# Performance work log

Measured on AMD Instinct MI355X. Metric: run time of the kernel, lower is better.

The kernel has to match this reference:

```python
import jax, jax.numpy as jnp
import numpy as np

S, B, D, H = 256, 32, 512, 512

def setup_inputs() -> dict:
    key = jax.random.key(0)
    ks = jax.random.split(key, 14)
    return {
        "x": jax.random.normal(ks[0], (S, B, D), jnp.float32),
        "hidden_prev": jax.random.normal(ks[1], (1, B, H), jnp.float32) * 0.1,
        "Z_state": jax.random.normal(ks[2], (1, B, H, D), jnp.float32) * 0.01,
        "F_state": jax.random.normal(ks[3], (1, B, H, D), jnp.float32) * 0.01,
        "wz_state": jax.random.normal(ks[4], (1, B, H), jnp.float32) * 0.01,
        "wf_state": jax.random.normal(ks[5], (1, B, H), jnp.float32) * 0.01,
        "bz_state": jax.random.normal(ks[6], (1, B, H), jnp.float32) * 0.01,
        "bf_state": jax.random.normal(ks[7], (1, B, H), jnp.float32) * 0.01,
        "wm_z": jax.random.normal(ks[8], (H, D), jnp.float32) * 0.1,
        "wm_f": jax.random.normal(ks[9], (H, D), jnp.float32) * 0.1,
        "wv_z": jax.random.normal(ks[10], (1, H), jnp.float32) * 0.1,
        "wv_f": jax.random.normal(ks[11], (1, H), jnp.float32) * 0.1,
        "bias_z": jax.random.normal(ks[12], (1, H), jnp.float32) * 0.1,
        "bias_f": jax.random.normal(ks[13], (1, H), jnp.float32) * 0.1,
    }

def reference(x, hidden_prev, Z_state, F_state, wz_state, wf_state, bz_state, bf_state,
              wm_z, wm_f, wv_z, wv_f, bias_z, bias_f):
    # Input projections for both gates, done once: [S,B,H]
    pre_z = jnp.einsum('sbd,hd->sbh', x, wm_z)
    pre_f = jnp.einsum('sbd,hd->sbh', x, wm_f)

    def step(carry, inp):
        cell, Z, Fm, wz, wf, bz, bf = carry
        x_t, pz, pf = inp  # [B,D], [B,H], [B,H]
        z = jnp.tanh(pz + wv_z * cell + bias_z)          # [B,H]
        f = jax.nn.sigmoid(pf + wv_f * cell + bias_f)    # [B,H]
        zf = (1.0 - f) * (1.0 - z * z)
        fz = (cell - z) * (1.0 - f) * f
        common = f + zf * wv_z + fz * wv_f
        # RTRL sensitivity updates (outer products over [B,H,D])
        Zn = common[..., None] * Z + zf[..., None] * x_t[:, None, :]
        Fn = common[..., None] * Fm + fz[..., None] * x_t[:, None, :]
        wzn = cell * zf + common * wz
        wfn = cell * fz + common * wf
        bzn = zf + common * bz
        bfn = fz + common * bf
        new_cell = cell * f + (1.0 - f) * z
        return (new_cell, Zn, Fn, wzn, wfn, bzn, bfn), new_cell

    carry0 = (hidden_prev[0], Z_state[0], F_state[0],
              wz_state[0], wf_state[0], bz_state[0], bf_state[0])
    carry, cells = jax.lax.scan(step, carry0, (x, pre_z, pre_f))
    new_cell, Zn, Fn, wzn, wfn, bzn, bfn = carry
    return (cells, new_cell[None], Zn[None], Fn[None],
            wzn[None], wfn[None], bzn[None], bfn[None])
```

## Files before the change

kernel.cpp:

```cpp
#include <hip/hip_runtime.h>
#include <math.h>

namespace {

typedef short short8 __attribute__((ext_vector_type(8)));
typedef float floatx4 __attribute__((ext_vector_type(4)));
typedef unsigned int uint32;
typedef unsigned short u16;
typedef unsigned long long u64;

constexpr int S = 256, B = 32, D = 512, H = 512;
constexpr int BH = B * H;
constexpr int M1 = S * B;
constexpr int WN = H * D;
constexpr int SBH = S * BH;

__device__ __forceinline__ int swz(int row, int col8) {
  return row * 64 + (col8 ^ ((row & 7) << 3));
}

__device__ __forceinline__ uint32 f2bf(float f) {
  uint32 x = __float_as_uint(f);
  return (x + 0x7fffu + ((x >> 16) & 1u)) >> 16;
}

__device__ __forceinline__ float fast_sigmoid(float x) {
  float e = __expf(-x);
  return __builtin_amdgcn_rcpf(1.0f + e);
}
__device__ __forceinline__ float fast_tanh(float x) {
  float e = __expf(-2.0f * x);
  return fmaf(2.0f, __builtin_amdgcn_rcpf(1.0f + e), -1.0f);
}

__global__ __launch_bounds__(256) void prep_kernel(
    const float* __restrict__ x, const float* __restrict__ wmz,
    const float* __restrict__ wmf, u16* __restrict__ XT,
    u16* __restrict__ wmzb, u16* __restrict__ wmfb) {
  __shared__ float lds[64][65];
  const int bid = blockIdx.x;
  if (bid < 1024) {
    const int b = bid >> 5;
    const int rem = bid & 31;
    const int d0 = (rem >> 2) * 64;
    const int s0 = (rem & 3) * 64;
    const int r = threadIdx.x >> 4;
    const int c4 = (threadIdx.x & 15) * 4;
#pragma unroll
    for (int p = 0; p < 4; ++p) {
      const int rr = r + p * 16;
      float4 v = *(const float4*)&x[(size_t)(s0 + rr) * (B * D) +
                                    (size_t)b * D + d0 + c4];
      lds[c4 + 0][rr] = v.x;
      lds[c4 + 1][rr] = v.y;
      lds[c4 + 2][rr] = v.z;
      lds[c4 + 3][rr] = v.w;
    }
    __syncthreads();
#pragma unroll
    for (int p = 0; p < 4; ++p) {
      const int dr = r + p * 16;
      const float v0 = lds[dr][c4 + 0];
      const float v1 = lds[dr][c4 + 1];
      const float v2 = lds[dr][c4 + 2];
      const float v3 = lds[dr][c4 + 3];
      u64 o = (u64)f2bf(v0) | ((u64)f2bf(v1) << 16) | ((u64)f2bf(v2) << 32) |
              ((u64)f2bf(v3) << 48);
      *(u64*)&XT[((size_t)b * D + d0 + dr) * S + s0 + c4] = o;
    }
  } else {
    int i = ((bid - 1024) * 256 + threadIdx.x) * 8;
    const float* src;
    u16* dst;
    int off;
    if (i < WN) {
      src = wmz; dst = wmzb; off = i;
    } else {
      src = wmf; dst = wmfb; off = i - WN;
    }
    float4 a = *(const float4*)&src[off];
    float4 b4 = *(const float4*)&src[off + 4];
    uint4 o;
    o.x = f2bf(a.x) | (f2bf(a.y) << 16);
    o.y = f2bf(a.z) | (f2bf(a.w) << 16);
    o.z = f2bf(b4.x) | (f2bf(b4.y) << 16);
    o.w = f2bf(b4.z) | (f2bf(b4.w) << 16);
    *(uint4*)&dst[off] = o;
  }
}

__global__ __launch_bounds__(256) void proj_gemm(
    const float* __restrict__ x, const u16* __restrict__ wmzb,
    const u16* __restrict__ wmfb, float2* __restrict__ pzf) {
  __shared__ u16 As[128 * 64];
  __shared__ u16 Bzs[64 * 64];
  __shared__ u16 Bfs[64 * 64];
  const int tid = threadIdx.x;
  const int m0 = blockIdx.x * 128;
  const int n0 = blockIdx.y * 64;
  const int w = tid >> 6, l = tid & 63;
  const int lr = l & 15, lg = l >> 4;
  floatx4 accz[2][4], accf[2][4];
#pragma unroll
  for (int m = 0; m < 2; ++m)
#pragma unroll
    for (int n = 0; n < 4; ++n) {
      accz[m][n] = 0;
      accf[m][n] = 0;
    }
  const int sr = tid >> 3;
  const int sc = (tid & 7) * 8;
  for (int k0 = 0; k0 < D; k0 += 64) {
    __syncthreads();
#pragma unroll
    for (int p = 0; p < 4; ++p) {
      const int r = sr + 32 * p;
      const float* xp = &x[(size_t)(m0 + r) * D + k0 + sc];
      float4 a = *(const float4*)xp;
      float4 b = *(const float4*)(xp + 4);
      uint4 o;
      o.x = f2bf(a.x) | (f2bf(a.y) << 16);
      o.y = f2bf(a.z) | (f2bf(a.w) << 16);
      o.z = f2bf(b.x) | (f2bf(b.y) << 16);
      o.w = f2bf(b.z) | (f2bf(b.w) << 16);
      *(uint4*)&As[swz(r, sc)] = o;
    }
#pragma unroll
    for (int p = 0; p < 2; ++p) {
      const int r = sr + 32 * p;
      *(short8*)&Bzs[swz(r, sc)] =
          *(const short8*)&wmzb[(size_t)(n0 + r) * D + k0 + sc];
      *(short8*)&Bfs[swz(r, sc)] =
          *(const short8*)&wmfb[(size_t)(n0 + r) * D + k0 + sc];
    }
    __syncthreads();
    __builtin_amdgcn_s_setprio(1);
#pragma unroll
    for (int kk = 0; kk < 2; ++kk) {
      const int kb = kk * 32 + lg * 8;
      short8 a0 = *(const short8*)&As[swz(32 * w + lr, kb)];
      short8 a1 = *(const short8*)&As[swz(32 * w + 16 + lr, kb)];
#pragma unroll
      for (int n = 0; n < 4; ++n) {
        short8 bz = *(const short8*)&Bzs[swz(16 * n + lr, kb)];
        short8 bf = *(const short8*)&Bfs[swz(16 * n + lr, kb)];
        accz[0][n] = __builtin_amdgcn_mfma_f32_16x16x32_bf16(a0, bz, accz[0][n], 0, 0, 0);
        accz[1][n] = __builtin_amdgcn_mfma_f32_16x16x32_bf16(a1, bz, accz[1][n], 0, 0, 0);
        accf[0][n] = __builtin_amdgcn_mfma_f32_16x16x32_bf16(a0, bf, accf[0][n], 0, 0, 0);
        accf[1][n] = __builtin_amdgcn_mfma_f32_16x16x32_bf16(a1, bf, accf[1][n], 0, 0, 0);
      }
    }
    __builtin_amdgcn_s_setprio(0);
  }
#pragma unroll
  for (int m = 0; m < 2; ++m)
#pragma unroll
    for (int n = 0; n < 4; ++n)
#pragma unroll
      for (int j = 0; j < 4; ++j) {
        int row = m0 + 32 * w + 16 * m + lg * 4 + j;
        int col = n0 + 16 * n + lr;
        pzf[(size_t)row * H + col] = make_float2(accz[m][n][j], accf[m][n][j]);
      }
}

#define STEP_BODY(J)                                                       \
    const float z = fast_tanh(fmaf(wvz, cell, pzv));                       \
    const float f = fast_sigmoid(fmaf(wvf, cell, pfv));                    \
    const float zf = (1.0f - f) * (1.0f - z * z);                          \
    const float fz = (cell - z) * (1.0f - f) * f;                          \
    const float common = f + zf * wvz + fz * wvf;                          \
    wz = fmaf(common, wz, cell * zf);                                      \
    wf = fmaf(common, wf, cell * fz);                                      \
    bz = fmaf(common, bz, zf);                                             \
    bf = fmaf(common, bf, fz);                                             \
    cell = fmaf(f, cell - z, z);                                           \
    const size_t ti = (size_t)(t0 + (J)) * BH;                             \
    cp[ti] = cell;                                                         \
    pz[ti] = make_float2(                                                  \
        __uint_as_float(f2bf(zf) | (f2bf(fz) << 16)), common);

#define STEP_L(J, Q)                                                       \
  {                                                                        \
    const float pzv = Q.x + bsz, pfv = Q.y + bsf;                          \
    Q = pz[(size_t)(t0 + 16 + (J)) * BH];                                  \
    STEP_BODY(J)                                                           \
  }

#define STEP_N(J, Q)                                                       \
  {                                                                        \
    const float pzv = Q.x + bsz, pfv = Q.y + bsf;                          \
    STEP_BODY(J)                                                           \
  }

__global__ __launch_bounds__(64, 1) void scan_fwd(
    const float* __restrict__ hidden_prev, const float* __restrict__ wz0,
    const float* __restrict__ wf0, const float* __restrict__ bz0,
    const float* __restrict__ bf0, const float* __restrict__ wvz_,
    const float* __restrict__ wvf_, const float* __restrict__ bsz_,
    const float* __restrict__ bsf_, float2* pzf_,
    float* __restrict__ out_cells, float* __restrict__ out_newcell,
    float* __restrict__ out_wzn, float* __restrict__ out_wfn,
    float* __restrict__ out_bzn, float* __restrict__ out_bfn) {
  const int bh = blockIdx.x * 64 + threadIdx.x;
  const int h = bh & (H - 1);
  float cell = hidden_prev[bh];
  float wz = wz0[bh], wf = wf0[bh], bz = bz0[bh], bf = bf0[bh];
  const float wvz = wvz_[h], wvf = wvf_[h], bsz = bsz_[h], bsf = bsf_[h];
  float2* pz = pzf_ + bh;
  float* cp = out_cells + bh;

  float2 q0 = pz[(size_t)0 * BH], q1 = pz[(size_t)1 * BH];
  float2 q2 = pz[(size_t)2 * BH], q3 = pz[(size_t)3 * BH];
  float2 q4 = pz[(size_t)4 * BH], q5 = pz[(size_t)5 * BH];
  float2 q6 = pz[(size_t)6 * BH], q7 = pz[(size_t)7 * BH];
  float2 q8 = pz[(size_t)8 * BH], q9 = pz[(size_t)9 * BH];
  float2 q10 = pz[(size_t)10 * BH], q11 = pz[(size_t)11 * BH];
  float2 q12 = pz[(size_t)12 * BH], q13 = pz[(size_t)13 * BH];
  float2 q14 = pz[(size_t)14 * BH], q15 = pz[(size_t)15 * BH];

  for (int t0 = 0; t0 < S - 16; t0 += 16) {
    STEP_L(0, q0)  STEP_L(1, q1)  STEP_L(2, q2)  STEP_L(3, q3)
    STEP_L(4, q4)  STEP_L(5, q5)  STEP_L(6, q6)  STEP_L(7, q7)
    STEP_L(8, q8)  STEP_L(9, q9)  STEP_L(10, q10) STEP_L(11, q11)
    STEP_L(12, q12) STEP_L(13, q13) STEP_L(14, q14) STEP_L(15, q15)
  }
  {
    const int t0 = S - 16;
    STEP_N(0, q0)  STEP_N(1, q1)  STEP_N(2, q2)  STEP_N(3, q3)
    STEP_N(4, q4)  STEP_N(5, q5)  STEP_N(6, q6)  STEP_N(7, q7)
    STEP_N(8, q8)  STEP_N(9, q9)  STEP_N(10, q10) STEP_N(11, q11)
    STEP_N(12, q12) STEP_N(13, q13) STEP_N(14, q14) STEP_N(15, q15)
  }
  out_newcell[bh] = cell;
  out_wzn[bh] = wz;
  out_wfn[bh] = wf;
  out_bzn[bh] = bz;
  out_bfn[bh] = bf;
}

__global__ __launch_bounds__(1024) void suffix_kernel(
    const float2* __restrict__ pzfc, u16* __restrict__ AzT,
    u16* __restrict__ AfT, float* __restrict__ P0_out) {
  __shared__ float prods[16][65];
  __shared__ uint32 tl[S * 65];
  const int bh_l = threadIdx.x & 63;
  const int c = threadIdx.x >> 6;
  const int bh = blockIdx.x * 64 + bh_l;
  const float2* p = pzfc + bh;
  float2 v[16];
#pragma unroll
  for (int i = 0; i < 16; ++i) v[i] = p[(size_t)(c * 16 + i) * BH];
  float L = 1.0f;
#pragma unroll
  for (int i = 0; i < 16; ++i) L *= v[i].y;
  prods[c][bh_l] = L;
  __syncthreads();
  float run = 1.0f;
#pragma unroll
  for (int cc = 1; cc < 16; ++cc)
    if (cc > c) run *= prods[cc][bh_l];
#pragma unroll
  for (int i = 15; i >= 0; --i) {
    const int t = c * 16 + i;
    const uint32 w32 = __float_as_uint(v[i].x);
    const float zf = __uint_as_float((w32 & 0xffffu) << 16);
    const float fz = __uint_as_float(w32 & 0xffff0000u);
    tl[t * 65 + bh_l] = f2bf(zf * run) | (f2bf(fz * run) << 16);
    run *= v[i].y;
  }
  if (c == 0) P0_out[bh] = run;
  __syncthreads();
  const size_t base = (size_t)blockIdx.x * 64 * S;
#pragma unroll
  for (int it = 0; it < 4; ++it) {
    const int qi = it * 1024 + threadIdx.x;
    const int r = qi >> 6;
    const int qt = (qi & 63) * 4;
    const uint32 a0 = tl[(qt + 0) * 65 + r];
    const uint32 a1 = tl[(qt + 1) * 65 + r];
    const uint32 a2 = tl[(qt + 2) * 65 + r];
    const uint32 a3 = tl[(qt + 3) * 65 + r];
    u64 lo = (u64)(a0 & 0xffffu) | ((u64)(a1 & 0xffffu) << 16) |
             ((u64)(a2 & 0xffffu) << 32) | ((u64)(a3 & 0xffffu) << 48);
    u64 hi = (u64)(a0 >> 16) | ((u64)(a1 >> 16) << 16) |
             ((u64)(a2 >> 16) << 32) | ((u64)(a3 >> 16) << 48);
    *(u64*)&AzT[base + (size_t)r * S + qt] = lo;
    *(u64*)&AfT[base + (size_t)r * S + qt] = hi;
  }
}

__global__ __launch_bounds__(256, 3) void out_gemm(
    const u16* __restrict__ AzT, const u16* __restrict__ AfT,
    const u16* __restrict__ XT, const float* __restrict__ P0,
    const float* __restrict__ Z0, const float* __restrict__ F0,
    float* __restrict__ Zn, float* __restrict__ Fn) {
  __shared__ u16 smem[2][(128 + 64) * 64];
  const int tid = threadIdx.x;
  const int h0 = blockIdx.x * 128;
  const int d0 = blockIdx.y * 64;
  const int bz = blockIdx.z;
  const int b = bz >> 1;
  const u16* A = ((bz & 1) ? AfT : AzT) + (size_t)b * H * S;
  const float* C0 = (bz & 1) ? F0 : Z0;
  float* Cn = (bz & 1) ? Fn : Zn;
  const u16* Xb = XT + (size_t)b * D * S;
  const int w = tid >> 6, l = tid & 63;
  const int lr = l & 15, lg = l >> 4;
  floatx4 acc[2][4];
#pragma unroll
  for (int m = 0; m < 2; ++m)
#pragma unroll
    for (int n = 0; n < 4; ++n) acc[m][n] = 0;
  const int sr = tid >> 3;
  const int sc = (tid & 7) * 8;

  short8 rA[4], rX[2];

#define OG_LOAD(T0)                                                        \
  {                                                                        \
    _Pragma("unroll") for (int p = 0; p < 4; ++p) {                        \
      const int r = sr + 32 * p;                                           \
      rA[p] = *(const short8*)&A[(size_t)(h0 + r) * S + (T0) + sc];        \
    }                                                                      \
    _Pragma("unroll") for (int p = 0; p < 2; ++p) {                        \
      const int r = sr + 32 * p;                                           \
      rX[p] = *(const short8*)&Xb[(size_t)(d0 + r) * S + (T0) + sc];       \
    }                                                                      \
  }

#define OG_WRITE(BUF)                                                      \
  {                                                                        \
    u16* As_ = smem[BUF];                                                  \
    u16* Xs_ = smem[BUF] + 128 * 64;                                       \
    _Pragma("unroll") for (int p = 0; p < 4; ++p) {                        \
      const int r = sr + 32 * p;                                           \
      *(short8*)&As_[swz(r, sc)] = rA[p];                                  \
    }                                                                      \
    _Pragma("unroll") for (int p = 0; p < 2; ++p) {                        \
      const int r = sr + 32 * p;                                           \
      *(short8*)&Xs_[swz(r, sc)] = rX[p];                                  \
    }                                                                      \
  }

#define OG_COMPUTE(BUF)                                                    \
  {                                                                        \
    const u16* As_ = smem[BUF];                                            \
    const u16* Xs_ = smem[BUF] + 128 * 64;                                 \
    __builtin_amdgcn_s_setprio(1);                                         \
    _Pragma("unroll") for (int kk = 0; kk < 2; ++kk) {                     \
      const int kb = kk * 32 + lg * 8;                                     \
      short8 a0 = *(const short8*)&As_[swz(32 * w + lr, kb)];              \
      short8 a1 = *(const short8*)&As_[swz(32 * w + 16 + lr, kb)];         \
      _Pragma("unroll") for (int n = 0; n < 4; ++n) {                      \
        short8 xf = *(const short8*)&Xs_[swz(16 * n + lr, kb)];            \
        acc[0][n] = __builtin_amdgcn_mfma_f32_16x16x32_bf16(a0, xf, acc[0][n], 0, 0, 0); \
        acc[1][n] = __builtin_amdgcn_mfma_f32_16x16x32_bf16(a1, xf, acc[1][n], 0, 0, 0); \
      }                                                                    \
    }                                                                      \
    __builtin_amdgcn_s_setprio(0);                                         \
  }

  OG_LOAD(0)
  OG_WRITE(0)
  __syncthreads();
  OG_LOAD(64)
  OG_COMPUTE(0)
  OG_WRITE(1)
  __syncthreads();
  OG_LOAD(128)
  OG_COMPUTE(1)
  OG_WRITE(0)
  __syncthreads();
  OG_LOAD(192)
  OG_COMPUTE(0)
  OG_WRITE(1)
  __syncthreads();

  float4 c0v[8];
  float p0v[8];
#pragma unroll
  for (int i = 0; i < 8; ++i) {
    const int id = i * 256 + tid;
    const int row = id >> 4;
    const int c4 = (id & 15) * 4;
    const int h = h0 + row;
    p0v[i] = P0[b * H + h];
    c0v[i] = *(const float4*)&C0[((size_t)b * H + h) * D + d0 + c4];
  }

  OG_COMPUTE(1)

  __syncthreads();
  float* eps = (float*)&smem[0][0];
#pragma unroll
  for (int m = 0; m < 2; ++m)
#pragma unroll
    for (int n = 0; n < 4; ++n)
#pragma unroll
      for (int j = 0; j < 4; ++j) {
        const int row = 32 * w + 16 * m + lg * 4 + j;
        eps[row * 68 + 16 * n + lr] = acc[m][n][j];
      }
  __syncthreads();
#pragma unroll
  for (int i = 0; i < 8; ++i) {
    const int id = i * 256 + tid;
    const int row = id >> 4;
    const int c4 = (id & 15) * 4;
    const int h = h0 + row;
    const size_t gi = ((size_t)b * H + h) * D + d0 + c4;
    const float4 a = *(const float4*)&eps[row * 68 + c4];
    float4 o;
    o.x = fmaf(p0v[i], c0v[i].x, a.x);
    o.y = fmaf(p0v[i], c0v[i].y, a.y);
    o.z = fmaf(p0v[i], c0v[i].z, a.z);
    o.w = fmaf(p0v[i], c0v[i].w, a.w);
    *(float4*)&Cn[gi] = o;
  }
#undef OG_LOAD
#undef OG_WRITE
#undef OG_COMPUTE
}

}

extern "C" void kernel_launch(void* const* d_in, const int* in_sizes, int n_in,
                              void* d_out, int out_size, void* d_ws,
                              size_t ws_size, hipStream_t stream) {
  const float* x = (const float*)d_in[0];
  const float* hidden_prev = (const float*)d_in[1];
  const float* Z_state = (const float*)d_in[2];
  const float* F_state = (const float*)d_in[3];
  const float* wz_state = (const float*)d_in[4];
  const float* wf_state = (const float*)d_in[5];
  const float* bz_state = (const float*)d_in[6];
  const float* bf_state = (const float*)d_in[7];
  const float* wm_z = (const float*)d_in[8];
  const float* wm_f = (const float*)d_in[9];
  const float* wv_z = (const float*)d_in[10];
  const float* wv_f = (const float*)d_in[11];
  const float* bias_z = (const float*)d_in[12];
  const float* bias_f = (const float*)d_in[13];

  float2* pzf = (float2*)d_ws;
  u16* AzT = (u16*)(pzf + SBH);
  u16* AfT = AzT + SBH;
  u16* XT = AfT + SBH;
  u16* wmzb = XT + SBH;
  u16* wmfb = wmzb + WN;
  float* P0 = (float*)(wmfb + WN);

  float* out = (float*)d_out;
  float* out_cells = out;
  float* out_newcell = out + SBH;
  float* out_Zn = out_newcell + BH;
  float* out_Fn = out_Zn + (size_t)BH * D;
  float* out_wzn = out_Fn + (size_t)BH * D;
  float* out_wfn = out_wzn + BH;
  float* out_bzn = out_wfn + BH;
  float* out_bfn = out_bzn + BH;

  prep_kernel<<<1024 + 256, 256, 0, stream>>>(x, wm_z, wm_f, XT, wmzb, wmfb);
  proj_gemm<<<dim3(M1 / 128, H / 64), 256, 0, stream>>>(x, wmzb, wmfb, pzf);
  scan_fwd<<<BH / 64, 64, 0, stream>>>(
      hidden_prev, wz_state, wf_state, bz_state, bf_state, wv_z, wv_f, bias_z,
      bias_f, pzf, out_cells, out_newcell, out_wzn, out_wfn, out_bzn,
      out_bfn);
  suffix_kernel<<<BH / 64, 1024, 0, stream>>>(pzf, AzT, AfT, P0);
  out_gemm<<<dim3(H / 128, D / 64, B * 2), 256, 0, stream>>>(
      AzT, AfT, XT, P0, Z_state, F_state, out_Zn, out_Fn);
}
```

Baseline: 101.9 us.

## Drop prep kernel: convert weights in GEMM, fuse x transpose into suffix kernel

Removes the separate prep kernel. proj_gemm now loads fp32 weights and converts them to bf16 in-kernel, and the x transpose-to-bf16 (XT) is folded into suffix_kernel, reusing its LDS through a union. The bf16 conversion switches to the packed __float22bfloat162_rn intrinsic, and the LDS transpose reads are rotated to reduce bank conflicts. This saves one launch and the bf16 weight staging buffers, but each proj_gemm block now re-reads and re-converts fp32 weights and suffix_kernel does extra work before its main phase.

```diff
diff --git a/kernel.cpp b/kernel.cpp
--- a/kernel.cpp
+++ b/kernel.cpp
@@ -1,4 +1,5 @@
 #include <hip/hip_runtime.h>
+#include <hip/hip_bf16.h>
 #include <math.h>
 
 namespace {
@@ -12,16 +13,17 @@
 constexpr int S = 256, B = 32, D = 512, H = 512;
 constexpr int BH = B * H;
 constexpr int M1 = S * B;
-constexpr int WN = H * D;
 constexpr int SBH = S * BH;
 
 __device__ __forceinline__ int swz(int row, int col8) {
   return row * 64 + (col8 ^ ((row & 7) << 3));
 }
 
-__device__ __forceinline__ uint32 f2bf(float f) {
-  uint32 x = __float_as_uint(f);
-  return (x + 0x7fffu + ((x >> 16) & 1u)) >> 16;
+__device__ __forceinline__ uint32 pkbf(float lo, float hi) {
+  __hip_bfloat162 h = __float22bfloat162_rn(make_float2(lo, hi));
+  uint32 r;
+  __builtin_memcpy(&r, &h, 4);
+  return r;
 }
 
 __device__ __forceinline__ float fast_sigmoid(float x) {
@@ -33,65 +35,9 @@
   return fmaf(2.0f, __builtin_amdgcn_rcpf(1.0f + e), -1.0f);
 }
 
-__global__ __launch_bounds__(256) void prep_kernel(
+__global__ __launch_bounds__(256) void proj_gemm(
     const float* __restrict__ x, const float* __restrict__ wmz,
-    const float* __restrict__ wmf, u16* __restrict__ XT,
-    u16* __restrict__ wmzb, u16* __restrict__ wmfb) {
-  __shared__ float lds[64][65];
-  const int bid = blockIdx.x;
-  if (bid < 1024) {
-    const int b = bid >> 5;
-    const int rem = bid & 31;
-    const int d0 = (rem >> 2) * 64;
-    const int s0 = (rem & 3) * 64;
-    const int r = threadIdx.x >> 4;
-    const int c4 = (threadIdx.x & 15) * 4;
-#pragma unroll
-    for (int p = 0; p < 4; ++p) {
-      const int rr = r + p * 16;
-      float4 v = *(const float4*)&x[(size_t)(s0 + rr) * (B * D) +
-                                    (size_t)b * D + d0 + c4];
-      lds[c4 + 0][rr] = v.x;
-      lds[c4 + 1][rr] = v.y;
-      lds[c4 + 2][rr] = v.z;
-      lds[c4 + 3][rr] = v.w;
-    }
-    __syncthreads();
-#pragma unroll
-    for (int p = 0; p < 4; ++p) {
-      const int dr = r + p * 16;
-      const float v0 = lds[dr][c4 + 0];
-      const float v1 = lds[dr][c4 + 1];
-      const float v2 = lds[dr][c4 + 2];
-      const float v3 = lds[dr][c4 + 3];
-      u64 o = (u64)f2bf(v0) | ((u64)f2bf(v1) << 16) | ((u64)f2bf(v2) << 32) |
-              ((u64)f2bf(v3) << 48);
-      *(u64*)&XT[((size_t)b * D + d0 + dr) * S + s0 + c4] = o;
-    }
-  } else {
-    int i = ((bid - 1024) * 256 + threadIdx.x) * 8;
-    const float* src;
-    u16* dst;
-    int off;
-    if (i < WN) {
-      src = wmz; dst = wmzb; off = i;
-    } else {
-      src = wmf; dst = wmfb; off = i - WN;
-    }
-    float4 a = *(const float4*)&src[off];
-    float4 b4 = *(const float4*)&src[off + 4];
-    uint4 o;
-    o.x = f2bf(a.x) | (f2bf(a.y) << 16);
-    o.y = f2bf(a.z) | (f2bf(a.w) << 16);
-    o.z = f2bf(b4.x) | (f2bf(b4.y) << 16);
-    o.w = f2bf(b4.z) | (f2bf(b4.w) << 16);
-    *(uint4*)&dst[off] = o;
-  }
-}
-
-__global__ __launch_bounds__(256) void proj_gemm(
-    const float* __restrict__ x, const u16* __restrict__ wmzb,
-    const u16* __restrict__ wmfb, float2* __restrict__ pzf) {
+    const float* __restrict__ wmf, float2* __restrict__ pzf) {
   __shared__ u16 As[128 * 64];
   __shared__ u16 Bzs[64 * 64];
   __shared__ u16 Bfs[64 * 64];
@@ -119,19 +65,33 @@
       float4 a = *(const float4*)xp;
       float4 b = *(const float4*)(xp + 4);
       uint4 o;
-      o.x = f2bf(a.x) | (f2bf(a.y) << 16);
-      o.y = f2bf(a.z) | (f2bf(a.w) << 16);
-      o.z = f2bf(b.x) | (f2bf(b.y) << 16);
-      o.w = f2bf(b.z) | (f2bf(b.w) << 16);
+      o.x = pkbf(a.x, a.y);
+      o.y = pkbf(a.z, a.w);
+      o.z = pkbf(b.x, b.y);
+      o.w = pkbf(b.z, b.w);
       *(uint4*)&As[swz(r, sc)] = o;
     }
 #pragma unroll
     for (int p = 0; p < 2; ++p) {
       const int r = sr + 32 * p;
-      *(short8*)&Bzs[swz(r, sc)] =
-          *(const short8*)&wmzb[(size_t)(n0 + r) * D + k0 + sc];
-      *(short8*)&Bfs[swz(r, sc)] =
-          *(const short8*)&wmfb[(size_t)(n0 + r) * D + k0 + sc];
+      const float* zp = &wmz[(size_t)(n0 + r) * D + k0 + sc];
+      float4 a = *(const float4*)zp;
+      float4 b = *(const float4*)(zp + 4);
+      uint4 o;
+      o.x = pkbf(a.x, a.y);
+      o.y = pkbf(a.z, a.w);
+      o.z = pkbf(b.x, b.y);
+      o.w = pkbf(b.z, b.w);
+      *(uint4*)&Bzs[swz(r, sc)] = o;
+      const float* fp = &wmf[(size_t)(n0 + r) * D + k0 + sc];
+      float4 c = *(const float4*)fp;
+      float4 d = *(const float4*)(fp + 4);
+      uint4 q;
+      q.x = pkbf(c.x, c.y);
+      q.y = pkbf(c.z, c.w);
+      q.z = pkbf(d.x, d.y);
+      q.w = pkbf(d.z, d.w);
+      *(uint4*)&Bfs[swz(r, sc)] = q;
     }
     __syncthreads();
     __builtin_amdgcn_s_setprio(1);
@@ -177,8 +137,7 @@
     cell = fmaf(f, cell - z, z);                                           \
     const size_t ti = (size_t)(t0 + (J)) * BH;                             \
     cp[ti] = cell;                                                         \
-    pz[ti] = make_float2(                                                  \
-        __uint_as_float(f2bf(zf) | (f2bf(fz) << 16)), common);
+    pz[ti] = make_float2(__uint_as_float(pkbf(zf, fz)), common);
 
 #define STEP_L(J, Q)                                                       \
   {                                                                        \
@@ -240,12 +199,51 @@
 }
 
 __global__ __launch_bounds__(1024) void suffix_kernel(
-    const float2* __restrict__ pzfc, u16* __restrict__ AzT,
-    u16* __restrict__ AfT, float* __restrict__ P0_out) {
-  __shared__ float prods[16][65];
-  __shared__ uint32 tl[S * 65];
-  const int bh_l = threadIdx.x & 63;
-  const int c = threadIdx.x >> 6;
+    const float2* __restrict__ pzfc, const float* __restrict__ x,
+    u16* __restrict__ XT, u16* __restrict__ AzT, u16* __restrict__ AfT,
+    float* __restrict__ P0_out) {
+  __shared__ union {
+    struct {
+      float prods[16][65];
+      uint32 tl[S * 65];
+    } s;
+    float xp[4][64][65];
+  } u;
+  const int tid = threadIdx.x;
+  const int bh_l = tid & 63;
+  const int c = tid >> 6;
+
+  {
+    const int team = tid >> 8;
+    const int tt = tid & 255;
+    const int tile = blockIdx.x * 4 + team;
+    const int b = tile >> 5;
+    const int rem = tile & 31;
+    const int d0 = (rem >> 2) * 64;
+    const int s0 = (rem & 3) * 64;
+    const int r = tt >> 4;
+    const int c4 = (tt & 15) * 4;
+#pragma unroll
+    for (int p = 0; p < 4; ++p) {
+      const int rr = r + p * 16;
+      float4 v = *(const float4*)&x[(size_t)(s0 + rr) * (B * D) +
+                                    (size_t)b * D + d0 + c4];
+      u.xp[team][c4 + 0][rr] = v.x;
+      u.xp[team][c4 + 1][rr] = v.y;
+      u.xp[team][c4 + 2][rr] = v.z;
+      u.xp[team][c4 + 3][rr] = v.w;
+    }
+    __syncthreads();
+#pragma unroll
+    for (int p = 0; p < 4; ++p) {
+      const int dr = r + p * 16;
+      u64 o = (u64)pkbf(u.xp[team][dr][c4 + 0], u.xp[team][dr][c4 + 1]) |
+              ((u64)pkbf(u.xp[team][dr][c4 + 2], u.xp[team][dr][c4 + 3]) << 32);
+      *(u64*)&XT[((size_t)b * D + d0 + dr) * S + s0 + c4] = o;
+    }
+  }
+  __syncthreads();
+
   const int bh = blockIdx.x * 64 + bh_l;
   const float2* p = pzfc + bh;
   float2 v[16];
@@ -254,37 +252,41 @@
   float L = 1.0f;
 #pragma unroll
   for (int i = 0; i < 16; ++i) L *= v[i].y;
-  prods[c][bh_l] = L;
+  u.s.prods[c][bh_l] = L;
   __syncthreads();
   float run = 1.0f;
 #pragma unroll
   for (int cc = 1; cc < 16; ++cc)
-    if (cc > c) run *= prods[cc][bh_l];
+    if (cc > c) run *= u.s.prods[cc][bh_l];
 #pragma unroll
   for (int i = 15; i >= 0; --i) {
     const int t = c * 16 + i;
     const uint32 w32 = __float_as_uint(v[i].x);
     const float zf = __uint_as_float((w32 & 0xffffu) << 16);
     const float fz = __uint_as_float(w32 & 0xffff0000u);
-    tl[t * 65 + bh_l] = f2bf(zf * run) | (f2bf(fz * run) << 16);
+    u.s.tl[t * 65 + bh_l] = pkbf(zf * run, fz * run);
     run *= v[i].y;
   }
   if (c == 0) P0_out[bh] = run;
   __syncthreads();
+
   const size_t base = (size_t)blockIdx.x * 64 * S;
+  const int rot = (bh_l >> 3) & 3;
 #pragma unroll
   for (int it = 0; it < 4; ++it) {
-    const int qi = it * 1024 + threadIdx.x;
+    const int qi = it * 1024 + tid;
     const int r = qi >> 6;
     const int qt = (qi & 63) * 4;
-    const uint32 a0 = tl[(qt + 0) * 65 + r];
-    const uint32 a1 = tl[(qt + 1) * 65 + r];
-    const uint32 a2 = tl[(qt + 2) * 65 + r];
-    const uint32 a3 = tl[(qt + 3) * 65 + r];
-    u64 lo = (u64)(a0 & 0xffffu) | ((u64)(a1 & 0xffffu) << 16) |
-             ((u64)(a2 & 0xffffu) << 32) | ((u64)(a3 & 0xffffu) << 48);
-    u64 hi = (u64)(a0 >> 16) | ((u64)(a1 >> 16) << 16) |
-             ((u64)(a2 >> 16) << 32) | ((u64)(a3 >> 16) << 48);
+    uint32 a[4];
+#pragma unroll
+    for (int m = 0; m < 4; ++m) {
+      const int k = (m + rot) & 3;
+      a[k] = u.s.tl[(qt + k) * 65 + r];
+    }
+    u64 lo = (u64)(a[0] & 0xffffu) | ((u64)(a[1] & 0xffffu) << 16) |
+             ((u64)(a[2] & 0xffffu) << 32) | ((u64)(a[3] & 0xffffu) << 48);
+    u64 hi = (u64)(a[0] >> 16) | ((u64)(a[1] >> 16) << 16) |
+             ((u64)(a[2] >> 16) << 32) | ((u64)(a[3] >> 16) << 48);
     *(u64*)&AzT[base + (size_t)r * S + qt] = lo;
     *(u64*)&AfT[base + (size_t)r * S + qt] = hi;
   }
@@ -447,9 +449,7 @@
   u16* AzT = (u16*)(pzf + SBH);
   u16* AfT = AzT + SBH;
   u16* XT = AfT + SBH;
-  u16* wmzb = XT + SBH;
-  u16* wmfb = wmzb + WN;
-  float* P0 = (float*)(wmfb + WN);
+  float* P0 = (float*)(XT + SBH);
 
   float* out = (float*)d_out;
   float* out_cells = out;
@@ -461,13 +461,12 @@
   float* out_bzn = out_wfn + BH;
   float* out_bfn = out_bzn + BH;
 
-  prep_kernel<<<1024 + 256, 256, 0, stream>>>(x, wm_z, wm_f, XT, wmzb, wmfb);
-  proj_gemm<<<dim3(M1 / 128, H / 64), 256, 0, stream>>>(x, wmzb, wmfb, pzf);
+  proj_gemm<<<dim3(M1 / 128, H / 64), 256, 0, stream>>>(x, wm_z, wm_f, pzf);
   scan_fwd<<<BH / 64, 64, 0, stream>>>(
       hidden_prev, wz_state, wf_state, bz_state, bf_state, wv_z, wv_f, bias_z,
       bias_f, pzf, out_cells, out_newcell, out_wzn, out_wfn, out_bzn,
       out_bfn);
-  suffix_kernel<<<BH / 64, 1024, 0, stream>>>(pzf, AzT, AfT, P0);
+  suffix_kernel<<<BH / 64, 1024, 0, stream>>>(pzf, x, XT, AzT, AfT, P0);
   out_gemm<<<dim3(H / 128, D / 64, B * 2), 256, 0, stream>>>(
       AzT, AfT, XT, P0, Z_state, F_state, out_Zn, out_Fn);
 }
```

Result: no change. 102.3 us (+0.4%).
